# Kernel optimization log

Measured on AMD Instinct MI355X. Metric: run time of the kernel, lower is better.

## Reference

```python
import jax, jax.numpy as jnp
import numpy as np
import math

B, C, H, W = 8, 512, 32, 32
ENC = 1024
L2 = 64
NH = 8
GROUPS = 32
EPS = 1e-5

def group_norm(x, gamma, beta):
    # x: (B, C, L) GroupNorm with 32 groups (float32)
    b, c, l = x.shape
    xg = x.reshape(b, GROUPS, (c // GROUPS) * l)
    mean = xg.mean(-1, keepdims=True)
    var = xg.var(-1, keepdims=True)
    xn = ((xg - mean) * jax.lax.rsqrt(var + EPS)).reshape(b, c, l)
    return xn * gamma[None, :, None] + beta[None, :, None]

def conv1x1(w, bias, x):
    # conv_nd(1, in, out, 1): w (out, in), x (B, in, L) -> (B, out, L)
    return jnp.einsum('oc,bcl->bol', w, x) + bias[None, :, None]

def setup_inputs() -> dict:
    key = jax.random.key(0)
    ks = jax.random.split(key, 16)
    s = lambda fan_in: 1.0 / math.sqrt(fan_in)
    inp = {
        'x': jax.random.normal(ks[0], (B, C, H, W), jnp.float32),
        'xf_out': jax.random.normal(ks[1], (B, ENC, L2), jnp.float32),
        'obj_class_embedding': jax.random.normal(ks[2], (B, ENC, L2), jnp.float32),
        'obj_bbox_embedding': jax.random.normal(ks[3], (B, ENC, L2), jnp.float32),
        'image_patch_bbox_embedding': jax.random.normal(ks[4], (B, ENC, H * W), jnp.float32),
        'key_padding_mask': jax.random.bernoulli(ks[5], 0.3, (B, L2)),
        'qkv_w': jax.random.normal(ks[6], (3 * C, C), jnp.float32) * s(C),
        'qkv_b': jnp.zeros((3 * C,), jnp.float32),
        'g_qkv': jnp.ones((C,), jnp.float32),
        'b_qkv': jnp.zeros((C,), jnp.float32),
        'lc_w': jax.random.normal(ks[7], (2 * C, ENC), jnp.float32) * s(ENC),
        'lc_b': jnp.zeros((2 * C,), jnp.float32),
        'lp_w': jax.random.normal(ks[8], (C, ENC), jnp.float32) * s(ENC),
        'lp_b': jnp.zeros((C,), jnp.float32),
        'g_obj': jnp.ones((ENC,), jnp.float32),
        'b_obj': jnp.zeros((ENC,), jnp.float32),
        'g_lpos': jnp.ones((C,), jnp.float32),
        'b_lpos': jnp.zeros((C,), jnp.float32),
        'g_ipos': jnp.ones((C,), jnp.float32),
        'b_ipos': jnp.zeros((C,), jnp.float32),
        # proj_out is zero-initialized in the original (zero_module); use random
        # weights so the projection math is exercised non-trivially.
        'proj_w': jax.random.normal(ks[9], (C, C), jnp.float32) * s(C),
        'proj_b': jnp.zeros((C,), jnp.float32),
    }
    return inp

def reference(x, xf_out, obj_class_embedding, obj_bbox_embedding,
              image_patch_bbox_embedding, key_padding_mask,
              qkv_w, qkv_b, g_qkv, b_qkv, lc_w, lc_b, lp_w, lp_b,
              g_obj, b_obj, g_lpos, b_lpos, g_ipos, b_ipos, proj_w, proj_b):
    b, c, h, w = x.shape
    L1 = h * w
    d = C // NH
    xf = x.reshape(b, c, L1)

    qkv = conv1x1(qkv_w, qkv_b, group_norm(xf, g_qkv, b_qkv))  # (B, 3C, L1)
    q, k, v = jnp.split(qkv, 3, axis=1)
    q = q.reshape(b * NH, d, L1)
    k = k.reshape(b * NH, d, L1)
    v = v.reshape(b * NH, d, L1)

    ipp = group_norm(conv1x1(lp_w, lp_b, image_patch_bbox_embedding), g_ipos, b_ipos)
    ipp = ipp.reshape(b * NH, d, L1)

    q_img = jnp.concatenate([q, ipp], axis=1)  # (B*H, 2d, L1)
    k_img = jnp.concatenate([k, ipp], axis=1)

    lpe = group_norm(conv1x1(lp_w, lp_b, obj_bbox_embedding), g_lpos, b_lpos)
    lpe = lpe.reshape(b * NH, d, L2)

    lce = (xf_out + group_norm(obj_class_embedding, g_obj, b_obj)) / 2
    kl, vl = jnp.split(conv1x1(lc_w, lc_b, lce), 2, axis=1)
    kl = kl.reshape(b * NH, d, L2)
    vl = vl.reshape(b * NH, d, L2)
    k_layout = jnp.concatenate([kl, lpe], axis=1)  # (B*H, 2d, L2)

    k_mix = jnp.concatenate([k_img, k_layout], axis=2)  # (B*H, 2d, L1+L2)
    v_mix = jnp.concatenate([v, vl], axis=2)             # (B*H, d, L1+L2)

    mask = jnp.concatenate([jnp.zeros((b, L1), bool), key_padding_mask], axis=1)  # (B, L1+L2)

    scale = 1.0 / math.sqrt(math.sqrt(2 * C // NH))
    attn = jnp.einsum('bct,bcs->bts', q_img * scale, k_mix * scale)  # (B*H, L1, L1+L2)
    attn = attn.reshape(b, NH, L1, L1 + L2)
    attn = jnp.where(mask[:, None, None, :], -jnp.inf, attn)
    attn = jax.nn.softmax(attn.astype(jnp.float32), axis=-1).astype(attn.dtype)
    attn = attn.reshape(b * NH, L1, L1 + L2)

    out = jnp.einsum('bts,bcs->bct', attn, v_mix).reshape(b, C, L1)
    hproj = conv1x1(proj_w, proj_b, out)
    return (xf + hproj).reshape(b, c, h, w)
```

## Files before the change

kernel.cpp:

```cpp
#include <hip/hip_runtime.h>
#include <math.h>

#define NB 8
#define NC 512
#define NL1 1024
#define NL2 64
#define NLKV 1088
#define NENC 1024
#define EPSV 1e-5f
#define SCALE2 0.08838834764831845f
#define SCALE2Q 0.12752425f
#define DEFER_THR 11.5415603f

typedef _Float16 half8 __attribute__((ext_vector_type(8)));
typedef _Float16 half4 __attribute__((ext_vector_type(4)));
typedef __fp16 fp16x2 __attribute__((ext_vector_type(2)));
typedef float f32x4 __attribute__((ext_vector_type(4)));
typedef float f32x16 __attribute__((ext_vector_type(16)));

__device__ __forceinline__ void gload16(const _Float16* g, _Float16* l) {
  __builtin_amdgcn_global_load_lds(
      (const __attribute__((address_space(1))) void*)g,
      (__attribute__((address_space(3))) void*)l, 16, 0, 0);
}

__device__ __forceinline__ unsigned int pkrtz(float a, float b) {
  union { fp16x2 hh; unsigned int uu; } cv;
  cv.hh = __builtin_amdgcn_cvt_pkrtz(a, b);
  return cv.uu;
}

__device__ __forceinline__ float fast_exp2(float x) {
  return __builtin_amdgcn_exp2f(x);
}

__global__ __launch_bounds__(256) void k_init(
    const float* __restrict__ x, const float* __restrict__ obj,
    float* __restrict__ xm, float* __restrict__ xr,
    float* __restrict__ om, float* __restrict__ orr,
    const float* __restrict__ qkv_w, _Float16* __restrict__ w16qkv,
    const float* __restrict__ lp_w, _Float16* __restrict__ w16lp,
    const float* __restrict__ proj_w, _Float16* __restrict__ w16proj,
    const float* __restrict__ lc_w, _Float16* __restrict__ w16lc)
{
  int bid = blockIdx.x;
  if (bid < 512) {
    const float* p; float* meanp; float* rstdp; int n, bg;
    if (bid < 256) {
      bg = bid;
      int b = bg >> 5, g = bg & 31;
      p = x + ((size_t)b * 512 + (size_t)g * 16) * 1024;
      n = 16 * 1024; meanp = xm; rstdp = xr;
    } else {
      bg = bid - 256;
      int b = bg >> 5, g = bg & 31;
      p = obj + ((size_t)b * 1024 + (size_t)g * 32) * 64;
      n = 32 * 64; meanp = om; rstdp = orr;
    }
    float s = 0.f, s2 = 0.f;
    for (int i = threadIdx.x; i < n; i += 256) { float v = p[i]; s += v; s2 += v * v; }
    #pragma unroll
    for (int o = 32; o > 0; o >>= 1) { s += __shfl_down(s, o); s2 += __shfl_down(s2, o); }
    __shared__ float rs[4], rq[4];
    int lane = threadIdx.x & 63, w = threadIdx.x >> 6;
    if (lane == 0) { rs[w] = s; rq[w] = s2; }
    __syncthreads();
    if (threadIdx.x == 0) {
      float S = rs[0] + rs[1] + rs[2] + rs[3];
      float Q = rq[0] + rq[1] + rq[2] + rq[3];
      float m = S / n;
      float v = Q / n - m * m;
      if (v < 0.f) v = 0.f;
      meanp[bg] = m;
      rstdp[bg] = rsqrtf(v + EPSV);
    }
  } else {
    int cb = bid - 512;
    const float* s; _Float16* d; int i4;
    if (cb < 768)        { s = qkv_w;  d = w16qkv;  i4 = cb * 256 + threadIdx.x; }
    else if (cb < 1280)  { s = lp_w;   d = w16lp;   i4 = (cb - 768) * 256 + threadIdx.x; }
    else if (cb < 1536)  { s = proj_w; d = w16proj; i4 = (cb - 1280) * 256 + threadIdx.x; }
    else                 { s = lc_w;   d = w16lc;   i4 = (cb - 1536) * 256 + threadIdx.x; }
    float4 v = *(const float4*)&s[(size_t)i4 * 4];
// ... 70 lines not shown
      }
    }
    __syncthreads();
    int tr = threadIdx.x >> 2, c16 = (threadIdx.x & 3) * 16;
    _Float16* dst = (which == 0 ? lceT : objT) + ((size_t)b * 64 + tr) * 1024 + e0 + c16;
    *(half8*)dst = *(half8*)&tile[tr][c16];
    *(half8*)(dst + 8) = *(half8*)&tile[tr][c16 + 8];
  }
}

#define MFMA_CORE(KTOT)                                                                  \
  f32x4 acc[4][4];                                                                       \
  _Pragma("unroll") for (int i_ = 0; i_ < 4; i_++)                                       \
      _Pragma("unroll") for (int j_ = 0; j_ < 4; j_++) acc[i_][j_] = (f32x4)0.f;         \
  {                                                                                      \
    const int rsub = lane >> 3, csrc = (lane & 7) ^ rsub;                                \
    const int NT_ = (KTOT) / 64;                                                         \
    _Pragma("unroll") for (int i = 0; i < 4; i++) {                                      \
      int seg = w * 4 + i;                                                               \
      int row = seg * 8 + rsub;                                                          \
      gload16(Abase + (size_t)(m0 + row) * (KTOT) + csrc * 8, ldsA + seg * 512);         \
      gload16(Bbase + (size_t)(n0 + row) * (KTOT) + csrc * 8, ldsB + seg * 512);         \
    }                                                                                    \
    __syncthreads();                                                                     \
    int cur_ = 0;                                                                        \
    for (int t_ = 0; t_ < NT_; t_++) {                                                   \
      if (t_ + 1 < NT_) {                                                                \
        _Float16* da_ = ldsA + ((cur_ ^ 1) << 13);                                       \
        _Float16* db_ = ldsB + ((cur_ ^ 1) << 13);                                       \
        int kt = (t_ + 1) * 64;                                                          \
        _Pragma("unroll") for (int i = 0; i < 4; i++) {                                  \
          int seg = w * 4 + i;                                                           \
          int row = seg * 8 + rsub;                                                      \
          gload16(Abase + (size_t)(m0 + row) * (KTOT) + kt + csrc * 8, da_ + seg * 512); \
          gload16(Bbase + (size_t)(n0 + row) * (KTOT) + kt + csrc * 8, db_ + seg * 512); \
        }                                                                                \
      }                                                                                  \
      const char* ra_ = (const char*)(ldsA + (cur_ << 13));                              \
      const char* rb_ = (const char*)(ldsB + (cur_ << 13));                              \
      _Pragma("unroll") for (int kk = 0; kk < 2; kk++) {                                 \
        half8 af[4], bf[4];                                                              \
        _Pragma("unroll") for (int mb = 0; mb < 4; mb++) {                               \
          int row = wm + mb * 16 + l15;                                                  \
          af[mb] = *(const half8*)(ra_ + row * 128 +                                     \
                                   ((kk * 64 + lg * 16) ^ ((row & 7) << 4)));            \
        }                                                                                \
        _Pragma("unroll") for (int nb = 0; nb < 4; nb++) {                               \
          int row = wn + nb * 16 + l15;                                                  \
          bf[nb] = *(const half8*)(rb_ + row * 128 +                                     \
                                   ((kk * 64 + lg * 16) ^ ((row & 7) << 4)));            \
        }                                                                                \
        _Pragma("unroll") for (int mb = 0; mb < 4; mb++)                                 \
            _Pragma("unroll") for (int nb = 0; nb < 4; nb++)                             \
                acc[mb][nb] = __builtin_amdgcn_mfma_f32_16x16x32_f16(af[mb], bf[nb],     \
                                                                    acc[mb][nb], 0, 0, 0);\
      }                                                                                  \
      __syncthreads();                                                                   \
      cur_ ^= 1;                                                                         \
    }                                                                                    \
  }

#define MFMA_CORE_N64(KTOT)                                                              \
  f32x4 acc[4][2];                                                                       \
  _Pragma("unroll") for (int i_ = 0; i_ < 4; i_++)                                       \
      _Pragma("unroll") for (int j_ = 0; j_ < 2; j_++) acc[i_][j_] = (f32x4)0.f;         \
  {                                                                                      \
    const int rsub = lane >> 3, csrc = (lane & 7) ^ rsub;                                \
    const int NT_ = (KTOT) / 64;                                                         \
    _Pragma("unroll") for (int i = 0; i < 4; i++) {                                      \
      int seg = w * 4 + i;                                                               \
      int row = seg * 8 + rsub;                                                          \
      gload16(Abase + (size_t)(m0 + row) * (KTOT) + csrc * 8, ldsA + seg * 512);         \
    }                                                                                    \
    _Pragma("unroll") for (int i = 0; i < 2; i++) {                                      \
      int seg = w * 2 + i;                                                               \
      int row = seg * 8 + rsub;                                                          \
      gload16(Bbase + (size_t)row * (KTOT) + csrc * 8, ldsB + seg * 512);                \
    }                                                                                    \
    __syncthreads();                                                                     \
    int cur_ = 0;                                                                        \
    for (int t_ = 0; t_ < NT_; t_++) {                                                   \
      if (t_ + 1 < NT_) {                                                                \
        _Float16* da_ = ldsA + ((cur_ ^ 1) << 13);                                       \
        _Float16* db_ = ldsB + ((cur_ ^ 1) << 12);                                       \
        int kt = (t_ + 1) * 64;                                                          \
        _Pragma("unroll") for (int i = 0; i < 4; i++) {                                  \
          int seg = w * 4 + i;                                                           \
          int row = seg * 8 + rsub;                                                      \
          gload16(Abase + (size_t)(m0 + row) * (KTOT) + kt + csrc * 8, da_ + seg * 512); \
        }                                                                                \
        _Pragma("unroll") for (int i = 0; i < 2; i++) {                                  \
          int seg = w * 2 + i;                                                           \
          int row = seg * 8 + rsub;                                                      \
          gload16(Bbase + (size_t)row * (KTOT) + kt + csrc * 8, db_ + seg * 512);        \
        }                                                                                \
      }                                                                                  \
      const char* ra_ = (const char*)(ldsA + (cur_ << 13));                              \
      const char* rb_ = (const char*)(ldsB + (cur_ << 12));                              \
      _Pragma("unroll") for (int kk = 0; kk < 2; kk++) {                                 \
        half8 af[4], bf[2];                                                              \
        _Pragma("unroll") for (int mb = 0; mb < 4; mb++) {                               \
          int row = wm + mb * 16 + l15;                                                  \
          af[mb] = *(const half8*)(ra_ + row * 128 +                                     \
                                   ((kk * 64 + lg * 16) ^ ((row & 7) << 4)));            \
        }                                                                                \
        _Pragma("unroll") for (int nb = 0; nb < 2; nb++) {                               \
          int row = wn + nb * 16 + l15;                                                  \
          bf[nb] = *(const half8*)(rb_ + row * 128 +                                     \
                                   ((kk * 64 + lg * 16) ^ ((row & 7) << 4)));            \
        }                                                                                \
        _Pragma("unroll") for (int mb = 0; mb < 4; mb++)                                 \
            _Pragma("unroll") for (int nb = 0; nb < 2; nb++)                             \
                acc[mb][nb] = __builtin_amdgcn_mfma_f32_16x16x32_f16(af[mb], bf[nb],     \
                                                                    acc[mb][nb], 0, 0, 0);\
      }                                                                                  \
      __syncthreads();                                                                   \
      cur_ ^= 1;                                                                         \
    }                                                                                    \
  }

__global__ __launch_bounds__(256) void k_mfma_big(
    const _Float16* __restrict__ w16qkv, const float* __restrict__ qkv_b,
    const _Float16* __restrict__ xhatT,
    const _Float16* __restrict__ w16lp, const float* __restrict__ lp_b,
    const _Float16* __restrict__ ipbeT,
    const _Float16* __restrict__ w16lc, const float* __restrict__ lc_b,
    const _Float16* __restrict__ lceT, const _Float16* __restrict__ objT,
    const float* __restrict__ g_lpos, const float* __restrict__ b_lpos,
    _Float16* __restrict__ qT, _Float16* __restrict__ kT, _Float16* __restrict__ vT,
    _Float16* __restrict__ ipp16)
{
  __shared__ _Float16 smem[32768];
  const int bid0 = blockIdx.x;
  const int bid = (bid0 < 608) ? (bid0 + 768) : (bid0 - 608);
  const int tid = threadIdx.x, lane = tid & 63, w = tid >> 6;
  const int l15 = lane & 15, lg = lane >> 4;

  if (bid < 768) {
    const int nt = bid & 7, tt = bid >> 3;
    const int mt = tt % 12, b = tt / 12;
    const int m0 = mt * 128, n0 = nt * 128;
    _Float16* ldsA = smem;
    _Float16* ldsB = smem + 16384;
    const _Float16* Abase = w16qkv;
    const _Float16* Bbase = xhatT + (size_t)b * 1024 * 512;
    const int wm = (w >> 1) * 64, wn = (w & 1) * 64;
    MFMA_CORE(512)

    char* tb = (char*)smem;
    if (m0 < 1024) {
      const bool isq = (m0 < 512);
      const float qs = isq ? SCALE2Q : 1.f;
      #pragma unroll
      for (int mb = 0; mb < 4; mb++) {
        #pragma unroll
        for (int r = 0; r < 4; r++) {
          int mcol = wm + mb * 16 + lg * 4 + r;
          float bia = qkv_b[m0 + mcol];
          #pragma unroll
          for (int nb = 0; nb < 4; nb++) {
            int trow = wn + nb * 16 + l15;
            float val = (acc[mb][nb][r] + bia) * qs;
            *(_Float16*)(tb + ((trow * 256 + mcol * 2) ^ ((trow & 7) << 4))) = (_Float16)val;
          }
        }
      }
      __syncthreads();
      #pragma unroll
      for (int it = 0; it < 8; it++) {
        int e = it * 256 + tid;
        int trow = e >> 4, seg = e & 15;
        half8 v = *(const half8*)(tb + ((trow * 256 + seg * 16) ^ ((trow & 7) << 4)));
        if (isq) {
          int mq = m0 + seg * 8, hh = mq >> 6, dc = mq & 63;
          *(half8*)(qT + (((size_t)b * 8 + hh) * 1024 + n0 + trow) * 128 + dc) = v;
        } else {
          int mk = m0 - 512 + seg * 8, hh = mk >> 6, dc = mk & 63;
          *(half8*)(kT + (((size_t)b * 8 + hh) * 1088 + n0 + trow) * 128 + dc) = v;
        }
      }
    } else {
      #pragma unroll
      for (int mb = 0; mb < 4; mb++) {
        #pragma unroll
        for (int r = 0; r < 4; r++) {
          int mrow = wm + mb * 16 + lg * 4 + r;
          float bia = qkv_b[m0 + mrow];
          #pragma unroll
          for (int nb = 0; nb < 4; nb++) {
            int tcol = wn + nb * 16 + l15;
            *(_Float16*)(tb + ((mrow * 256 + tcol * 2) ^ ((mrow & 7) << 4))) =
                (_Float16)(acc[mb][nb][r] + bia);
          }
        }
      }
      __syncthreads();
      #pragma unroll
      for (int it = 0; it < 8; it++) {
        int e = it * 256 + tid;
        int mrow = e >> 4, seg = e & 15;
        half8 v = *(const half8*)(tb + ((mrow * 256 + seg * 16) ^ ((mrow & 7) << 4)));
        int mv = m0 - 1024 + mrow, hh = mv >> 6, dc = mv & 63;
        *(half8*)(vT + (((size_t)b * 8 + hh) * 64 + dc) * 1088 + n0 + seg * 8) = v;
      }
    }
  } else if (bid < 1280) {
    const int local = bid - 768;
    const int nt = local & 15, mt = (local >> 4) & 3, b = local >> 6;
    const int m0 = mt * 128, n0 = nt * 64;
    _Float16* ldsA = smem;
    _Float16* ldsB = smem + 16384;
    const _Float16* Abase = w16lp;
    const _Float16* Bbase = ipbeT + (size_t)b * 1024 * 1024 + (size_t)n0 * 1024;
    const int wm = (w >> 1) * 64, wn = (w & 1) * 32;
    MFMA_CORE_N64(1024)
    #pragma unroll
    for (int mb = 0; mb < 4; mb++) {
      #pragma unroll
      for (int r = 0; r < 4; r++) {
        int m = m0 + wm + mb * 16 + lg * 4 + r;
        float bia = lp_b[m];
        #pragma unroll
        for (int nb = 0; nb < 2; nb++) {
          int t = n0 + wn + nb * 16 + l15;
          ipp16[((size_t)b * NC + m) * NL1 + t] = (_Float16)(acc[mb][nb][r] + bia);
        }
      }
    }
  } else {
    const int local = bid - 1280;
    const int mt = local % 12, b = local / 12;
    const bool islc = (mt < 8);
    const int m0 = (islc ? mt : mt - 8) * 128;
    _Float16* ldsA = smem;
    _Float16* ldsB = smem + 16384;
    float (*red_s)[4] = (float(*)[4])(smem + 24576);
    float (*red_q)[4] = (float(*)[4])(smem + 24608);
    const _Float16* Abase = islc ? w16lc : w16lp;
    const float* bias = islc ? lc_b : lp_b;
    const _Float16* Bbase = (islc ? lceT : objT) + (size_t)b * 64 * 1024;
    const int wm = (w >> 1) * 64, wn = (w & 1) * 32;
    MFMA_CORE_N64(1024)

    if (islc) {
      #pragma unroll
      for (int mb = 0; mb < 4; mb++) {
        #pragma unroll
        for (int r = 0; r < 4; r++) {
          int m = m0 + wm + mb * 16 + lg * 4 + r;
          float bia = bias[m];
          #pragma unroll
          for (int nb = 0; nb < 2; nb++) {
            int l = wn + nb * 16 + l15;
// ... 43 lines not shown
      #pragma unroll
      for (int mb = 0; mb < 4; mb++) {
        float S = red_s[wbase][mb] + red_s[wbase + 1][mb];
        float Q = red_q[wbase][mb] + red_q[wbase + 1][mb];
        float mean = S * (1.f / 1024.f);
        float var = Q * (1.f / 1024.f) - mean * mean;
        if (var < 0.f) var = 0.f;
        float rstd = rsqrtf(var + EPSV);
        #pragma unroll
        for (int r = 0; r < 4; r++) {
          int c = m0 + wm + mb * 16 + lg * 4 + r;
          float ga = g_lpos[c] * rstd;
          float be = b_lpos[c] - mean * ga;
          int hh = c >> 6, dc = c & 63;
          #pragma unroll
          for (int nb = 0; nb < 2; nb++) {
            int l = wn + nb * 16 + l15;
            float xn = vals[mb][nb][r] * ga + be;
            kT[(((size_t)b * 8 + hh) * 1088 + 1024 + l) * 128 + 64 + dc] = (_Float16)xn;
          }
        }
      }
    }
  }
}

__global__ __launch_bounds__(256) void k_mfma_proj(
    const _Float16* __restrict__ Abase, const float* __restrict__ bias,
    const _Float16* __restrict__ Ball, const float* __restrict__ xin,
    float* __restrict__ out)
{
  __shared__ _Float16 smem[24576];
  _Float16* ldsA = smem;
  _Float16* ldsB = smem + 16384;
  const int b = blockIdx.z, mt = blockIdx.y, nt = blockIdx.x;
  const int m0 = mt * 128, n0 = nt * 64;
  const _Float16* Bbase = Ball + (size_t)b * 1024 * 512 + (size_t)n0 * 512;
  const int tid = threadIdx.x, lane = tid & 63, w = tid >> 6;
  const int l15 = lane & 15, lg = lane >> 4;
  const int wm = (w >> 1) * 64, wn = (w & 1) * 32;
  MFMA_CORE_N64(512)
  #pragma unroll
  for (int mb = 0; mb < 4; mb++) {
    #pragma unroll
    for (int r = 0; r < 4; r++) {
      int m = m0 + wm + mb * 16 + lg * 4 + r;
      float bia = bias[m];
      #pragma unroll
      for (int nb = 0; nb < 2; nb++) {
        int t = n0 + wn + nb * 16 + l15;
        size_t idx = ((size_t)b * NC + m) * NL1 + t;
        out[idx] = xin[idx] + acc[mb][nb][r] + bia;
      }
    }
  }
}

__global__ __launch_bounds__(256) void k_ipp_fuse(
    const _Float16* __restrict__ raw,
    const float* __restrict__ gm, const float* __restrict__ gb,
    _Float16* __restrict__ qT, _Float16* __restrict__ kT)
{
  const int g = blockIdx.x, b = blockIdx.y;
  const int tid = threadIdx.x;
  const _Float16* p = raw + ((size_t)b * 512 + (size_t)g * 16) * 1024;
  const int t0 = tid * 4;

  float4 v[16];
  float s = 0.f, s2 = 0.f;
  #pragma unroll
  for (int c = 0; c < 16; c++) {
    half4 hv = *(const half4*)&p[(size_t)c * 1024 + t0];
// ... 34 lines not shown
    #pragma unroll
    for (int c = 0; c < 8; c++) {
      float4 vc = v[c];
      float e = (j == 0) ? vc.x : (j == 1) ? vc.y : (j == 2) ? vc.z : vc.w;
      float xn = e * ga[c] + be[c];
      k0[c] = (_Float16)xn;
      q0[c] = (_Float16)(SCALE2Q * xn);
    }
    #pragma unroll
    for (int c = 8; c < 16; c++) {
      float4 vc = v[c];
      float e = (j == 0) ? vc.x : (j == 1) ? vc.y : (j == 2) ? vc.z : vc.w;
      float xn = e * ga[c] + be[c];
      k1[c - 8] = (_Float16)xn;
      q1[c - 8] = (_Float16)(SCALE2Q * xn);
    }
    _Float16* qd = qT + (bh * 1024 + t) * 128 + 64 + dcb;
    _Float16* kd = kT + (bh * 1088 + t) * 128 + 64 + dcb;
    *(half8*)qd = q0; *(half8*)(qd + 8) = q1;
    *(half8*)kd = k0; *(half8*)(kd + 8) = k1;
  }
}

__global__ __launch_bounds__(256) void k_attn_mfma(
    const _Float16* __restrict__ qT, const _Float16* __restrict__ kT,
    const _Float16* __restrict__ vT, const int* __restrict__ mask,
    _Float16* __restrict__ attnT)
{
  const int x = blockIdx.x & 7;
  const int k = blockIdx.x >> 3;
  const int bh = x + ((k >> 3) << 3);
  const int qt = k & 7;
  const int b = bh >> 3, h = bh & 7;
  const int tid = threadIdx.x;
  const int lane = tid & 63;
  const int w = tid >> 6;
  const int l31 = lane & 31;
  const int hi = lane >> 5;

  __shared__ _Float16 KsB[2 * 64 * 128];
  __shared__ _Float16 VtB[2 * 64 * 64];

  const int q = qt * 128 + w * 32 + l31;

  half8 aq[8];
  {
    const _Float16* qp = qT + ((size_t)bh * 1024 + q) * 128 + hi * 8;
    #pragma unroll
    for (int kst = 0; kst < 8; kst++) aq[kst] = *(const half8*)(qp + kst * 16);
  }

  unsigned int mbits = 0;
  {
    const int* mp = mask + b * 64;
    #pragma unroll
    for (int sb = 0; sb < 2; sb++) {
      #pragma unroll
      for (int reg = 0; reg < 16; reg++) {
        int s = sb * 32 + (reg & 3) + 8 * (reg >> 2) + 4 * hi;
        if (mp[s]) mbits |= 1u << (sb * 16 + reg);
      }
    }
  }

  f32x16 O0 = (f32x16)0.f, O1 = (f32x16)0.f;
  float m_run = -INFINITY, l_run = 0.f;

  const int kxor = (l31 & 7) << 4;
  const int ksrow_off = lane >> 4;
  const int kcsrc_base = lane & 15;
  const int vdc_off = lane >> 3;
  const int vcsrc_base = lane & 7;

#define STAGE_KV(T, KD, VD)                                                          \
  {                                                                                  \
    const int s0_ = (T) * 64;                                                        \
    _Pragma("unroll") for (int r = 0; r < 4; r++) {                                  \
      int seg = r * 4 + w;                                                           \
      int srow = seg * 4 + ksrow_off;                                                \
      int csrc = kcsrc_base ^ (srow & 7);                                            \
      gload16(kT + ((size_t)bh * 1088 + s0_ + srow) * 128 + csrc * 8, (KD) + seg * 512); \
    }                                                                                \
    _Pragma("unroll") for (int r = 0; r < 2; r++) {                                  \
      int seg = r * 4 + w;                                                           \
      int dc = seg * 8 + vdc_off;                                                    \
      int csrc = vcsrc_base ^ (dc & 7);                                              \
      gload16(vT + ((size_t)bh * 64 + dc) * 1088 + s0_ + csrc * 8, (VD) + seg * 512);  \
    }                                                                                \
  }

  STAGE_KV(0, KsB, VtB)
  asm volatile("s_waitcnt vmcnt(0)" ::: "memory");
  __builtin_amdgcn_s_barrier();

  int cur = 0;
  for (int t = 0; t < 17; t++) {
    if (t < 16) {
      _Float16* kd = KsB + ((cur ^ 1) << 13);
      _Float16* vd = VtB + ((cur ^ 1) << 12);
      STAGE_KV(t + 1, kd, vd)
    }
    const char* ksb = (const char*)(KsB + (cur << 13));
    const char* vtb = (const char*)(VtB + (cur << 12));

    f32x16 sc0 = (f32x16)0.f, sc1 = (f32x16)0.f;
    __builtin_amdgcn_s_setprio(1);
    #pragma unroll
    for (int kst = 0; kst < 8; kst++) {
      half8 kf0 = *(const half8*)(ksb + ((l31 * 256 + kst * 32 + hi * 16) ^ kxor));
      half8 kf1 = *(const half8*)(ksb + (((32 + l31) * 256 + kst * 32 + hi * 16) ^ kxor));
      sc0 = __builtin_amdgcn_mfma_f32_32x32x16_f16(kf0, aq[kst], sc0, 0, 0, 0);
      sc1 = __builtin_amdgcn_mfma_f32_32x32x16_f16(kf1, aq[kst], sc1, 0, 0, 0);
    }
    __builtin_amdgcn_s_setprio(0);

    if (t == 16) {
      #pragma unroll
      for (int i = 0; i < 16; i++) {
        if ((mbits >> i) & 1)        sc0[i] = -INFINITY;
        if ((mbits >> (16 + i)) & 1) sc1[i] = -INFINITY;
      }
    }

    float mx;
    {
      float a0 = fmaxf(fmaxf(sc0[0], sc0[1]), sc0[2]);
      float a1 = fmaxf(fmaxf(sc0[3], sc0[4]), sc0[5]);
      float a2 = fmaxf(fmaxf(sc0[6], sc0[7]), sc0[8]);
      float a3 = fmaxf(fmaxf(sc0[9], sc0[10]), sc0[11]);
      float a4 = fmaxf(fmaxf(sc0[12], sc0[13]), sc0[14]);
      float a5 = fmaxf(fmaxf(sc0[15], sc1[0]), sc1[1]);
      float a6 = fmaxf(fmaxf(sc1[2], sc1[3]), sc1[4]);
      float a7 = fmaxf(fmaxf(sc1[5], sc1[6]), sc1[7]);
      float a8 = fmaxf(fmaxf(sc1[8], sc1[9]), sc1[10]);
      float a9 = fmaxf(fmaxf(sc1[11], sc1[12]), sc1[13]);
      float aa = fmaxf(sc1[14], sc1[15]);
      float b0 = fmaxf(fmaxf(a0, a1), a2);
      float b1 = fmaxf(fmaxf(a3, a4), a5);
      float b2 = fmaxf(fmaxf(a6, a7), a8);
      float b3 = fmaxf(a9, aa);
      mx = fmaxf(fmaxf(b0, b1), fmaxf(b2, b3));
    }
    mx = fmaxf(mx, __shfl_xor(mx, 32));
    if (__all(mx <= m_run + DEFER_THR)) {
      float sum = 0.f;
      #pragma unroll
      for (int i = 0; i < 16; i++) { float p = fast_exp2(sc0[i] - m_run); sc0[i] = p; sum += p; }
      #pragma unroll
      for (int i = 0; i < 16; i++) { float p = fast_exp2(sc1[i] - m_run); sc1[i] = p; sum += p; }
      sum += __shfl_xor(sum, 32);
      l_run += sum;
    } else {
      float m_new = fmaxf(m_run, mx);
      float alpha = fast_exp2(m_run - m_new);
      float sum = 0.f;
      #pragma unroll
      for (int i = 0; i < 16; i++) { float p = fast_exp2(sc0[i] - m_new); sc0[i] = p; sum += p; }
      #pragma unroll
      for (int i = 0; i < 16; i++) { float p = fast_exp2(sc1[i] - m_new); sc1[i] = p; sum += p; }
      sum += __shfl_xor(sum, 32);
      l_run = l_run * alpha + sum;
      m_run = m_new;
      #pragma unroll
      for (int i = 0; i < 16; i++) { O0[i] *= alpha; O1[i] *= alpha; }
    }

    __builtin_amdgcn_s_setprio(1);
    #pragma unroll
    for (int sb = 0; sb < 2; sb++) {
      #pragma unroll
      for (int k2 = 0; k2 < 2; k2++) {
        const int kst = sb * 2 + k2;
        unsigned int pa0, pa1, pb0, pb1;
        if (sb == 0) {
          pa0 = pkrtz(sc0[8 * k2 + 0], sc0[8 * k2 + 1]);
          pa1 = pkrtz(sc0[8 * k2 + 2], sc0[8 * k2 + 3]);
          pb0 = pkrtz(sc0[8 * k2 + 4], sc0[8 * k2 + 5]);
          pb1 = pkrtz(sc0[8 * k2 + 6], sc0[8 * k2 + 7]);
        } else {
          pa0 = pkrtz(sc1[8 * k2 + 0], sc1[8 * k2 + 1]);
          pa1 = pkrtz(sc1[8 * k2 + 2], sc1[8 * k2 + 3]);
          pb0 = pkrtz(sc1[8 * k2 + 4], sc1[8 * k2 + 5]);
          pb1 = pkrtz(sc1[8 * k2 + 6], sc1[8 * k2 + 7]);
        }
        unsigned int keep0 = hi ? pb0 : pa0, keep1 = hi ? pb1 : pa1;
        unsigned int send0 = hi ? pa0 : pb0, send1 = hi ? pa1 : pb1;
        unsigned int recv0 = (unsigned int)__shfl_xor((int)send0, 32);
        unsigned int recv1 = (unsigned int)__shfl_xor((int)send1, 32);
        union { unsigned int u[4]; half8 hh; } pf;
        pf.u[0] = hi ? recv0 : keep0;
        pf.u[1] = hi ? recv1 : keep1;
        pf.u[2] = hi ? keep0 : recv0;
        pf.u[3] = hi ? keep1 : recv1;

        half8 vf0 = *(const half8*)(vtb + ((l31 * 128 + kst * 32 + hi * 16) ^ kxor));
        half8 vf1 = *(const half8*)(vtb + (((32 + l31) * 128 + kst * 32 + hi * 16) ^ kxor));
        O0 = __builtin_amdgcn_mfma_f32_32x32x16_f16(vf0, pf.hh, O0, 0, 0, 0);
        O1 = __builtin_amdgcn_mfma_f32_32x32x16_f16(vf1, pf.hh, O1, 0, 0, 0);
      }
    }
    __builtin_amdgcn_s_setprio(0);

    asm volatile("s_waitcnt vmcnt(0)" ::: "memory");
    __builtin_amdgcn_s_barrier();
    cur ^= 1;
  }

  float inv = 1.f / l_run;
  _Float16* op = attnT + ((size_t)b * 1024 + q) * 512 + h * 64;
  #pragma unroll
  for (int i = 0; i < 16; i += 2) {
    int dc = (i & 3) + 8 * (i >> 2) + 4 * hi;
    unsigned int c0 = pkrtz(O0[i] * inv, O0[i + 1] * inv);
    unsigned int c1 = pkrtz(O1[i] * inv, O1[i + 1] * inv);
    *(unsigned int*)(op + dc) = c0;
    *(unsigned int*)(op + 32 + dc) = c1;
  }
}

extern "C" void kernel_launch(void* const* d_in, const int* in_sizes, int n_in,
                              void* d_out, int out_size, void* d_ws, size_t ws_size,
                              hipStream_t stream) {
  const float* x         = (const float*)d_in[0];
  const float* xf_out    = (const float*)d_in[1];
  const float* obj_class = (const float*)d_in[2];
  const float* obj_bbox  = (const float*)d_in[3];
  const float* ipbe      = (const float*)d_in[4];
  const int*   mask      = (const int*)d_in[5];
// ... 19 lines not shown
  _Float16* qT      = f16b;
  _Float16* kT      = qT + 8388608;
  _Float16* vT      = kT + 8912896;
  _Float16* xhatT   = vT + 4456448;
  _Float16* ipbeT   = xhatT + 4194304;
  _Float16* attnT   = ipbeT + 8388608;
  _Float16* w16qkv  = attnT + 4194304;
  _Float16* w16lp   = w16qkv + 786432;
  _Float16* w16proj = w16lp + 524288;
  _Float16* w16lc   = w16proj + 262144;
  _Float16* lceT    = w16lc + 1048576;
  _Float16* objT    = lceT + 524288;
  _Float16* ipp16   = objT + 524288;
  float* st = (float*)(ipp16 + 4194304);
  float* xm = st, * xr = st + 256, * om = st + 512, * orr = st + 768;

  dim3 blk(256);
  k_init<<<dim3(3072), blk, 0, stream>>>(x, obj_class, xm, xr, om, orr,
                                         qkv_w, w16qkv, lp_w, w16lp, proj_w, w16proj, lc_w, w16lc);
  k_prep<<<dim3(3328), blk, 0, stream>>>(x, xm, xr, g_qkv, b_qkv, xhatT,
                                         ipbe, ipbeT,
                                         xf_out, obj_class, obj_bbox, om, orr, g_obj, b_obj,
                                         lceT, objT);
  k_mfma_big<<<dim3(1376), blk, 0, stream>>>(w16qkv, qkv_b, xhatT,
                                             w16lp, lp_b, ipbeT,
                                             w16lc, lc_b, lceT, objT,
                                             g_lpos, b_lpos,
                                             qT, kT, vT, ipp16);
  k_ipp_fuse<<<dim3(32, 8), blk, 0, stream>>>(ipp16, g_ipos, b_ipos, qT, kT);
  k_attn_mfma<<<dim3(512), blk, 0, stream>>>(qT, kT, vT, mask, attnT);
  k_mfma_proj<<<dim3(16, 4, 8), blk, 0, stream>>>(w16proj, proj_b, attnT, x, out);
}
```

Baseline: 138.2 us.

## Retile GEMMs and attention, pipeline LDS loads with vmcnt waits

```diff
diff --git a/kernel.cpp b/kernel.cpp
--- a/kernel.cpp
+++ b/kernel.cpp
@@ -17,6 +17,7 @@
 typedef __fp16 fp16x2 __attribute__((ext_vector_type(2)));
 typedef float f32x4 __attribute__((ext_vector_type(4)));
 typedef float f32x16 __attribute__((ext_vector_type(16)));
+typedef unsigned int uint32x2 __attribute__((ext_vector_type(2)));
 
 __device__ __forceinline__ void gload16(const _Float16* g, _Float16* l) {
   __builtin_amdgcn_global_load_lds(
@@ -45,7 +46,7 @@
 {
   int bid = blockIdx.x;
   if (bid < 512) {
-    const float* p; float* meanp; float* rstdp; int n, bg;
+    const float* p; float* meanp; float* rstdp; int n4, n, bg;
     if (bid < 256) {
       bg = bid;
       int b = bg >> 5, g = bg & 31;
@@ -57,8 +58,13 @@
       p = obj + ((size_t)b * 1024 + (size_t)g * 32) * 64;
       n = 32 * 64; meanp = om; rstdp = orr;
     }
+    n4 = n >> 2;
     float s = 0.f, s2 = 0.f;
-    for (int i = threadIdx.x; i < n; i += 256) { float v = p[i]; s += v; s2 += v * v; }
+    for (int i = threadIdx.x; i < n4; i += 256) {
+      float4 v = ((const float4*)p)[i];
+      s += v.x + v.y + v.z + v.w;
+      s2 += v.x * v.x + v.y * v.y + v.z * v.z + v.w * v.w;
+    }
     #pragma unroll
     for (int o = 32; o > 0; o >>= 1) { s += __shfl_down(s, o); s2 += __shfl_down(s2, o); }
     __shared__ float rs[4], rq[4];
@@ -175,7 +181,6 @@
       gload16(Abase + (size_t)(m0 + row) * (KTOT) + csrc * 8, ldsA + seg * 512);         \
       gload16(Bbase + (size_t)(n0 + row) * (KTOT) + csrc * 8, ldsB + seg * 512);         \
     }                                                                                    \
-    __syncthreads();                                                                     \
     int cur_ = 0;                                                                        \
     for (int t_ = 0; t_ < NT_; t_++) {                                                   \
       if (t_ + 1 < NT_) {                                                                \
@@ -188,7 +193,11 @@
           gload16(Abase + (size_t)(m0 + row) * (KTOT) + kt + csrc * 8, da_ + seg * 512); \
           gload16(Bbase + (size_t)(n0 + row) * (KTOT) + kt + csrc * 8, db_ + seg * 512); \
         }                                                                                \
+        asm volatile("s_waitcnt vmcnt(8)" ::: "memory");                                 \
+      } else {                                                                           \
+        asm volatile("s_waitcnt vmcnt(0)" ::: "memory");                                 \
       }                                                                                  \
+      __builtin_amdgcn_s_barrier();                                                      \
       const char* ra_ = (const char*)(ldsA + (cur_ << 13));                              \
       const char* rb_ = (const char*)(ldsB + (cur_ << 13));                              \
       _Pragma("unroll") for (int kk = 0; kk < 2; kk++) {                                 \
@@ -208,7 +217,7 @@
                 acc[mb][nb] = __builtin_amdgcn_mfma_f32_16x16x32_f16(af[mb], bf[nb],     \
                                                                     acc[mb][nb], 0, 0, 0);\
       }                                                                                  \
-      __syncthreads();                                                                   \
+      __builtin_amdgcn_s_barrier();                                                      \
       cur_ ^= 1;                                                                         \
     }                                                                                    \
   }
@@ -230,7 +239,6 @@
       int row = seg * 8 + rsub;                                                          \
       gload16(Bbase + (size_t)row * (KTOT) + csrc * 8, ldsB + seg * 512);                \
     }                                                                                    \
-    __syncthreads();                                                                     \
     int cur_ = 0;                                                                        \
     for (int t_ = 0; t_ < NT_; t_++) {                                                   \
       if (t_ + 1 < NT_) {                                                                \
@@ -247,7 +255,11 @@
           int row = seg * 8 + rsub;                                                      \
           gload16(Bbase + (size_t)row * (KTOT) + kt + csrc * 8, db_ + seg * 512);        \
         }                                                                                \
+        asm volatile("s_waitcnt vmcnt(6)" ::: "memory");                                 \
+      } else {                                                                           \
+        asm volatile("s_waitcnt vmcnt(0)" ::: "memory");                                 \
       }                                                                                  \
+      __builtin_amdgcn_s_barrier();                                                      \
       const char* ra_ = (const char*)(ldsA + (cur_ << 13));                              \
       const char* rb_ = (const char*)(ldsB + (cur_ << 12));                              \
       _Pragma("unroll") for (int kk = 0; kk < 2; kk++) {                                 \
@@ -267,7 +279,7 @@
                 acc[mb][nb] = __builtin_amdgcn_mfma_f32_16x16x32_f16(af[mb], bf[nb],     \
                                                                     acc[mb][nb], 0, 0, 0);\
       }                                                                                  \
-      __syncthreads();                                                                   \
+      __builtin_amdgcn_s_barrier();                                                      \
       cur_ ^= 1;                                                                         \
     }                                                                                    \
   }
@@ -285,88 +297,18 @@
 {
   __shared__ _Float16 smem[32768];
   const int bid0 = blockIdx.x;
-  const int bid = (bid0 < 608) ? (bid0 + 768) : (bid0 - 608);
   const int tid = threadIdx.x, lane = tid & 63, w = tid >> 6;
   const int l15 = lane & 15, lg = lane >> 4;
 
-  if (bid < 768) {
-    const int nt = bid & 7, tt = bid >> 3;
-    const int mt = tt % 12, b = tt / 12;
+  if (bid0 < 256) {
+    const int nt = bid0 & 7, mt = (bid0 >> 3) & 3, b = bid0 >> 5;
     const int m0 = mt * 128, n0 = nt * 128;
     _Float16* ldsA = smem;
     _Float16* ldsB = smem + 16384;
-    const _Float16* Abase = w16qkv;
-    const _Float16* Bbase = xhatT + (size_t)b * 1024 * 512;
+    const _Float16* Abase = w16lp;
+    const _Float16* Bbase = ipbeT + (size_t)b * 1024 * 1024;
     const int wm = (w >> 1) * 64, wn = (w & 1) * 64;
-    MFMA_CORE(512)
-
-    char* tb = (char*)smem;
-    if (m0 < 1024) {
-      const bool isq = (m0 < 512);
-      const float qs = isq ? SCALE2Q : 1.f;
-      #pragma unroll
-      for (int mb = 0; mb < 4; mb++) {
-        #pragma unroll
-        for (int r = 0; r < 4; r++) {
-          int mcol = wm + mb * 16 + lg * 4 + r;
-          float bia = qkv_b[m0 + mcol];
-          #pragma unroll
-          for (int nb = 0; nb < 4; nb++) {
-            int trow = wn + nb * 16 + l15;
-            float val = (acc[mb][nb][r] + bia) * qs;
-            *(_Float16*)(tb + ((trow * 256 + mcol * 2) ^ ((trow & 7) << 4))) = (_Float16)val;
-          }
-        }
-      }
-      __syncthreads();
-      #pragma unroll
-      for (int it = 0; it < 8; it++) {
-        int e = it * 256 + tid;
-        int trow = e >> 4, seg = e & 15;
-        half8 v = *(const half8*)(tb + ((trow * 256 + seg * 16) ^ ((trow & 7) << 4)));
-        if (isq) {
-          int mq = m0 + seg * 8, hh = mq >> 6, dc = mq & 63;
-          *(half8*)(qT + (((size_t)b * 8 + hh) * 1024 + n0 + trow) * 128 + dc) = v;
-        } else {
-          int mk = m0 - 512 + seg * 8, hh = mk >> 6, dc = mk & 63;
-          *(half8*)(kT + (((size_t)b * 8 + hh) * 1088 + n0 + trow) * 128 + dc) = v;
-        }
-      }
-    } else {
-      #pragma unroll
-      for (int mb = 0; mb < 4; mb++) {
-        #pragma unroll
-        for (int r = 0; r < 4; r++) {
-          int mrow = wm + mb * 16 + lg * 4 + r;
-          float bia = qkv_b[m0 + mrow];
-          #pragma unroll
-          for (int nb = 0; nb < 4; nb++) {
-            int tcol = wn + nb * 16 + l15;
-            *(_Float16*)(tb + ((mrow * 256 + tcol * 2) ^ ((mrow & 7) << 4))) =
-                (_Float16)(acc[mb][nb][r] + bia);
-          }
-        }
-      }
-      __syncthreads();
-      #pragma unroll
-      for (int it = 0; it < 8; it++) {
-        int e = it * 256 + tid;
-        int mrow = e >> 4, seg = e & 15;
-        half8 v = *(const half8*)(tb + ((mrow * 256 + seg * 16) ^ ((mrow & 7) << 4)));
-        int mv = m0 - 1024 + mrow, hh = mv >> 6, dc = mv & 63;
-        *(half8*)(vT + (((size_t)b * 8 + hh) * 64 + dc) * 1088 + n0 + seg * 8) = v;
-      }
-    }
-  } else if (bid < 1280) {
-    const int local = bid - 768;
-    const int nt = local & 15, mt = (local >> 4) & 3, b = local >> 6;
-    const int m0 = mt * 128, n0 = nt * 64;
-    _Float16* ldsA = smem;
-    _Float16* ldsB = smem + 16384;
-    const _Float16* Abase = w16lp;
-    const _Float16* Bbase = ipbeT + (size_t)b * 1024 * 1024 + (size_t)n0 * 1024;
-    const int wm = (w >> 1) * 64, wn = (w & 1) * 32;
-    MFMA_CORE_N64(1024)
+    MFMA_CORE(1024)
     #pragma unroll
     for (int mb = 0; mb < 4; mb++) {
       #pragma unroll
@@ -374,14 +316,14 @@
         int m = m0 + wm + mb * 16 + lg * 4 + r;
         float bia = lp_b[m];
         #pragma unroll
-        for (int nb = 0; nb < 2; nb++) {
+        for (int nb = 0; nb < 4; nb++) {
           int t = n0 + wn + nb * 16 + l15;
           ipp16[((size_t)b * NC + m) * NL1 + t] = (_Float16)(acc[mb][nb][r] + bia);
         }
       }
     }
-  } else {
-    const int local = bid - 1280;
+  } else if (bid0 < 352) {
+    const int local = bid0 - 256;
     const int mt = local % 12, b = local / 12;
     const bool islc = (mt < 8);
     const int m0 = (islc ? mt : mt - 8) * 128;
@@ -471,6 +413,75 @@
         }
       }
     }
+  } else {
+    const int bid = bid0 - 352;
+    const int nt = bid & 7, tt = bid >> 3;
+    const int mt = tt % 12, b = tt / 12;
+    const int m0 = mt * 128, n0 = nt * 128;
+    _Float16* ldsA = smem;
+    _Float16* ldsB = smem + 16384;
+    const _Float16* Abase = w16qkv;
+    const _Float16* Bbase = xhatT + (size_t)b * 1024 * 512;
+    const int wm = (w >> 1) * 64, wn = (w & 1) * 64;
+    MFMA_CORE(512)
+
+    char* tb = (char*)smem;
+    if (m0 < 1024) {
+      const bool isq = (m0 < 512);
+      const float qs = isq ? SCALE2Q : 1.f;
+      #pragma unroll
+      for (int mb = 0; mb < 4; mb++) {
+        #pragma unroll
+        for (int r = 0; r < 4; r++) {
+          int mcol = wm + mb * 16 + lg * 4 + r;
+          float bia = qkv_b[m0 + mcol];
+          #pragma unroll
+          for (int nb = 0; nb < 4; nb++) {
+            int trow = wn + nb * 16 + l15;
+            float val = (acc[mb][nb][r] + bia) * qs;
+            *(_Float16*)(tb + ((trow * 256 + mcol * 2) ^ ((trow & 7) << 4))) = (_Float16)val;
+          }
+        }
+      }
+      __syncthreads();
+      #pragma unroll
+      for (int it = 0; it < 8; it++) {
+        int e = it * 256 + tid;
+        int trow = e >> 4, seg = e & 15;
+        half8 v = *(const half8*)(tb + ((trow * 256 + seg * 16) ^ ((trow & 7) << 4)));
+        if (isq) {
+          int mq = m0 + seg * 8, hh = mq >> 6, dc = mq & 63;
+          *(half8*)(qT + (((size_t)b * 8 + hh) * 1024 + n0 + trow) * 128 + dc) = v;
+        } else {
+          int mk = m0 - 512 + seg * 8, hh = mk >> 6, dc = mk & 63;
+          *(half8*)(kT + (((size_t)b * 8 + hh) * 1088 + n0 + trow) * 128 + dc) = v;
+        }
+      }
+    } else {
+      #pragma unroll
+      for (int mb = 0; mb < 4; mb++) {
+        #pragma unroll
+        for (int r = 0; r < 4; r++) {
+          int mrow = wm + mb * 16 + lg * 4 + r;
+          float bia = qkv_b[m0 + mrow];
+          #pragma unroll
+          for (int nb = 0; nb < 4; nb++) {
+            int tcol = wn + nb * 16 + l15;
+            *(_Float16*)(tb + ((mrow * 256 + tcol * 2) ^ ((mrow & 7) << 4))) =
+                (_Float16)(acc[mb][nb][r] + bia);
+          }
+        }
+      }
+      __syncthreads();
+      #pragma unroll
+      for (int it = 0; it < 8; it++) {
+        int e = it * 256 + tid;
+        int mrow = e >> 4, seg = e & 15;
+        half8 v = *(const half8*)(tb + ((mrow * 256 + seg * 16) ^ ((mrow & 7) << 4)));
+        int mv = m0 - 1024 + mrow, hh = mv >> 6, dc = mv & 63;
+        *(half8*)(vT + (((size_t)b * 8 + hh) * 64 + dc) * 1088 + n0 + seg * 8) = v;
+      }
+    }
   }
 }
 
@@ -479,16 +490,16 @@
     const _Float16* __restrict__ Ball, const float* __restrict__ xin,
     float* __restrict__ out)
 {
-  __shared__ _Float16 smem[24576];
+  __shared__ _Float16 smem[32768];
   _Float16* ldsA = smem;
   _Float16* ldsB = smem + 16384;
   const int b = blockIdx.z, mt = blockIdx.y, nt = blockIdx.x;
-  const int m0 = mt * 128, n0 = nt * 64;
-  const _Float16* Bbase = Ball + (size_t)b * 1024 * 512 + (size_t)n0 * 512;
+  const int m0 = mt * 128, n0 = nt * 128;
+  const _Float16* Bbase = Ball + (size_t)b * 1024 * 512;
   const int tid = threadIdx.x, lane = tid & 63, w = tid >> 6;
   const int l15 = lane & 15, lg = lane >> 4;
-  const int wm = (w >> 1) * 64, wn = (w & 1) * 32;
-  MFMA_CORE_N64(512)
+  const int wm = (w >> 1) * 64, wn = (w & 1) * 64;
+  MFMA_CORE(512)
   #pragma unroll
   for (int mb = 0; mb < 4; mb++) {
     #pragma unroll
@@ -496,7 +507,7 @@
       int m = m0 + wm + mb * 16 + lg * 4 + r;
       float bia = bias[m];
       #pragma unroll
-      for (int nb = 0; nb < 2; nb++) {
+      for (int nb = 0; nb < 4; nb++) {
         int t = n0 + wn + nb * 16 + l15;
         size_t idx = ((size_t)b * NC + m) * NL1 + t;
         out[idx] = xin[idx] + acc[mb][nb][r] + bia;
@@ -577,15 +588,14 @@
   }
 }
 
-__global__ __launch_bounds__(256) void k_attn_mfma(
+__global__ __launch_bounds__(512, 1) void k_attn_mfma(
     const _Float16* __restrict__ qT, const _Float16* __restrict__ kT,
     const _Float16* __restrict__ vT, const int* __restrict__ mask,
     _Float16* __restrict__ attnT)
 {
-  const int x = blockIdx.x & 7;
-  const int k = blockIdx.x >> 3;
-  const int bh = x + ((k >> 3) << 3);
-  const int qt = k & 7;
+  const int bid = blockIdx.x;
+  const int bh = bid & 63;
+  const int qt = bid >> 6;
   const int b = bh >> 3, h = bh & 7;
   const int tid = threadIdx.x;
   const int lane = tid & 63;
@@ -593,10 +603,10 @@
   const int l31 = lane & 31;
   const int hi = lane >> 5;
 
-  __shared__ _Float16 KsB[2 * 64 * 128];
-  __shared__ _Float16 VtB[2 * 64 * 64];
-
-  const int q = qt * 128 + w * 32 + l31;
+  __shared__ _Float16 KsB[2 * 128 * 128];
+  __shared__ _Float16 VtB[3 * 64 * 128];
+
+  const int q = qt * 256 + w * 32 + l31;
 
   half8 aq[8];
   {
@@ -622,143 +632,156 @@
   float m_run = -INFINITY, l_run = 0.f;
 
   const int kxor = (l31 & 7) << 4;
-  const int ksrow_off = lane >> 4;
-  const int kcsrc_base = lane & 15;
-  const int vdc_off = lane >> 3;
-  const int vcsrc_base = lane & 7;
+  const int row_off = lane >> 4;
+  const int blk_base = lane & 15;
 
 #define STAGE_KV(T, KD, VD)                                                          \
   {                                                                                  \
-    const int s0_ = (T) * 64;                                                        \
+    const int s0_ = (T) * 128;                                                       \
     _Pragma("unroll") for (int r = 0; r < 4; r++) {                                  \
-      int seg = r * 4 + w;                                                           \
-      int srow = seg * 4 + ksrow_off;                                                \
-      int csrc = kcsrc_base ^ (srow & 7);                                            \
+      int seg = r * 8 + w;                                                           \
+      int srow = seg * 4 + row_off;                                                  \
+      int csrc = blk_base ^ (srow & 7);                                              \
       gload16(kT + ((size_t)bh * 1088 + s0_ + srow) * 128 + csrc * 8, (KD) + seg * 512); \
     }                                                                                \
     _Pragma("unroll") for (int r = 0; r < 2; r++) {                                  \
-      int seg = r * 4 + w;                                                           \
-      int dc = seg * 8 + vdc_off;                                                    \
-      int csrc = vcsrc_base ^ (dc & 7);                                              \
+      int seg = r * 8 + w;                                                           \
+      int dc = seg * 4 + row_off;                                                    \
+      int csrc = blk_base ^ (dc & 7);                                                \
       gload16(vT + ((size_t)bh * 64 + dc) * 1088 + s0_ + csrc * 8, (VD) + seg * 512);  \
     }                                                                                \
   }
+
+#define XHALF_FMAX(OUTV, INV)                                                        \
+  { unsigned int xi_ = __float_as_uint(INV);                                         \
+    uint32x2 xr_ = __builtin_amdgcn_permlane32_swap(xi_, xi_, false, false);         \
+    OUTV = fmaxf(__uint_as_float(xr_.x), __uint_as_float(xr_.y)); }
+#define XHALF_ADD(OUTV, INV)                                                         \
+  { unsigned int xi_ = __float_as_uint(INV);                                         \
+    uint32x2 xr_ = __builtin_amdgcn_permlane32_swap(xi_, xi_, false, false);         \
+    OUTV = __uint_as_float(xr_.x) + __uint_as_float(xr_.y); }
+
+#define MAX32(OUTV, P0, P1)                                                          \
+  { float a0 = fmaxf(fmaxf(P0[0], P0[1]), P0[2]);                                    \
+    float a1 = fmaxf(fmaxf(P0[3], P0[4]), P0[5]);                                    \
+    float a2 = fmaxf(fmaxf(P0[6], P0[7]), P0[8]);                                    \
+    float a3 = fmaxf(fmaxf(P0[9], P0[10]), P0[11]);                                  \
+    float a4 = fmaxf(fmaxf(P0[12], P0[13]), P0[14]);                                 \
+    float a5 = fmaxf(fmaxf(P0[15], P1[0]), P1[1]);                                   \
+    float a6 = fmaxf(fmaxf(P1[2], P1[3]), P1[4]);                                    \
+    float a7 = fmaxf(fmaxf(P1[5], P1[6]), P1[7]);                                    \
+    float a8 = fmaxf(fmaxf(P1[8], P1[9]), P1[10]);                                   \
+    float a9 = fmaxf(fmaxf(P1[11], P1[12]), P1[13]);                                 \
+    float aa = fmaxf(P1[14], P1[15]);                                                \
+    float b0 = fmaxf(fmaxf(a0, a1), a2);                                             \
+    float b1 = fmaxf(fmaxf(a3, a4), a5);                                             \
+    float b2 = fmaxf(fmaxf(a6, a7), a8);                                             \
+    float b3 = fmaxf(a9, aa);                                                        \
+    OUTV = fmaxf(fmaxf(b0, b1), fmaxf(b2, b3)); }
+
+#define EXP16(P, M, SUM)                                                             \
+  _Pragma("unroll") for (int i = 0; i < 16; i++) {                                   \
+    float p_ = fast_exp2(P[i] - (M)); P[i] = p_; SUM += p_; }
+
+#define PACK_G(PFU, SC, K2)                                                          \
+  { unsigned int pa0 = pkrtz(SC[8 * (K2) + 0], SC[8 * (K2) + 1]);                    \
+    unsigned int pa1 = pkrtz(SC[8 * (K2) + 2], SC[8 * (K2) + 3]);                    \
+    unsigned int pb0 = pkrtz(SC[8 * (K2) + 4], SC[8 * (K2) + 5]);                    \
+    unsigned int pb1 = pkrtz(SC[8 * (K2) + 6], SC[8 * (K2) + 7]);                    \
+    uint32x2 r0_ = __builtin_amdgcn_permlane32_swap(pa0, pb0, false, false);         \
+    uint32x2 r1_ = __builtin_amdgcn_permlane32_swap(pa1, pb1, false, false);         \
+    PFU.u[0] = r0_.x; PFU.u[1] = r1_.x; PFU.u[2] = r0_.y; PFU.u[3] = r1_.y; }
 
   STAGE_KV(0, KsB, VtB)
   asm volatile("s_waitcnt vmcnt(0)" ::: "memory");
   __builtin_amdgcn_s_barrier();
 
-  int cur = 0;
-  for (int t = 0; t < 17; t++) {
-    if (t < 16) {
-      _Float16* kd = KsB + ((cur ^ 1) << 13);
-      _Float16* vd = VtB + ((cur ^ 1) << 12);
-      STAGE_KV(t + 1, kd, vd)
-    }
-    const char* ksb = (const char*)(KsB + (cur << 13));
-    const char* vtb = (const char*)(VtB + (cur << 12));
+  for (int t = 0; t <= 8; t++) {
+    if (t < 8) {
+      STAGE_KV(t + 1, KsB + ((t + 1) & 1) * 16384, VtB + ((t + 1) % 3) * 8192)
+    }
+    const char* ksb_ = (const char*)(KsB + (t & 1) * 16384);
 
     f32x16 sc0 = (f32x16)0.f, sc1 = (f32x16)0.f;
+    f32x16 sc2 = (f32x16)0.f, sc3 = (f32x16)0.f;
+    const bool full = (t < 8);
     __builtin_amdgcn_s_setprio(1);
     #pragma unroll
     for (int kst = 0; kst < 8; kst++) {
-      half8 kf0 = *(const half8*)(ksb + ((l31 * 256 + kst * 32 + hi * 16) ^ kxor));
-      half8 kf1 = *(const half8*)(ksb + (((32 + l31) * 256 + kst * 32 + hi * 16) ^ kxor));
+      half8 kf0 = *(const half8*)(ksb_ + ((l31 * 256 + kst * 32 + hi * 16) ^ kxor));
+      half8 kf1 = *(const half8*)(ksb_ + (((32 + l31) * 256 + kst * 32 + hi * 16) ^ kxor));
       sc0 = __builtin_amdgcn_mfma_f32_32x32x16_f16(kf0, aq[kst], sc0, 0, 0, 0);
       sc1 = __builtin_amdgcn_mfma_f32_32x32x16_f16(kf1, aq[kst], sc1, 0, 0, 0);
+      if (full) {
+        half8 kf2 = *(const half8*)(ksb_ + (((64 + l31) * 256 + kst * 32 + hi * 16) ^ kxor));
+        half8 kf3 = *(const half8*)(ksb_ + (((96 + l31) * 256 + kst * 32 + hi * 16) ^ kxor));
+        sc2 = __builtin_amdgcn_mfma_f32_32x32x16_f16(kf2, aq[kst], sc2, 0, 0, 0);
+        sc3 = __builtin_amdgcn_mfma_f32_32x32x16_f16(kf3, aq[kst], sc3, 0, 0, 0);
+      }
     }
     __builtin_amdgcn_s_setprio(0);
 
-    if (t == 16) {
+    if (!full) {
       #pragma unroll
       for (int i = 0; i < 16; i++) {
         if ((mbits >> i) & 1)        sc0[i] = -INFINITY;
         if ((mbits >> (16 + i)) & 1) sc1[i] = -INFINITY;
-      }
-    }
-
-    float mx;
-    {
-      float a0 = fmaxf(fmaxf(sc0[0], sc0[1]), sc0[2]);
-      float a1 = fmaxf(fmaxf(sc0[3], sc0[4]), sc0[5]);
-      float a2 = fmaxf(fmaxf(sc0[6], sc0[7]), sc0[8]);
-      float a3 = fmaxf(fmaxf(sc0[9], sc0[10]), sc0[11]);
-      float a4 = fmaxf(fmaxf(sc0[12], sc0[13]), sc0[14]);
-      float a5 = fmaxf(fmaxf(sc0[15], sc1[0]), sc1[1]);
-      float a6 = fmaxf(fmaxf(sc1[2], sc1[3]), sc1[4]);
-      float a7 = fmaxf(fmaxf(sc1[5], sc1[6]), sc1[7]);
-      float a8 = fmaxf(fmaxf(sc1[8], sc1[9]), sc1[10]);
-      float a9 = fmaxf(fmaxf(sc1[11], sc1[12]), sc1[13]);
-      float aa = fmaxf(sc1[14], sc1[15]);
-      float b0 = fmaxf(fmaxf(a0, a1), a2);
-      float b1 = fmaxf(fmaxf(a3, a4), a5);
-      float b2 = fmaxf(fmaxf(a6, a7), a8);
-      float b3 = fmaxf(a9, aa);
-      mx = fmaxf(fmaxf(b0, b1), fmaxf(b2, b3));
-    }
-    mx = fmaxf(mx, __shfl_xor(mx, 32));
+        sc2[i] = -INFINITY;
+        sc3[i] = -INFINITY;
+      }
+    }
+
+    float mx01, mx23, mx;
+    MAX32(mx01, sc0, sc1)
+    if (full) { MAX32(mx23, sc2, sc3) mx = fmaxf(mx01, mx23); }
+    else mx = mx01;
+    XHALF_FMAX(mx, mx)
     if (__all(mx <= m_run + DEFER_THR)) {
       float sum = 0.f;
-      #pragma unroll
-      for (int i = 0; i < 16; i++) { float p = fast_exp2(sc0[i] - m_run); sc0[i] = p; sum += p; }
-      #pragma unroll
-      for (int i = 0; i < 16; i++) { float p = fast_exp2(sc1[i] - m_run); sc1[i] = p; sum += p; }
-      sum += __shfl_xor(sum, 32);
+      EXP16(sc0, m_run, sum)
+      EXP16(sc1, m_run, sum)
+      if (full) { EXP16(sc2, m_run, sum) EXP16(sc3, m_run, sum) }
+      XHALF_ADD(sum, sum)
       l_run += sum;
     } else {
       float m_new = fmaxf(m_run, mx);
       float alpha = fast_exp2(m_run - m_new);
       float sum = 0.f;
-      #pragma unroll
-      for (int i = 0; i < 16; i++) { float p = fast_exp2(sc0[i] - m_new); sc0[i] = p; sum += p; }
-      #pragma unroll
-      for (int i = 0; i < 16; i++) { float p = fast_exp2(sc1[i] - m_new); sc1[i] = p; sum += p; }
-      sum += __shfl_xor(sum, 32);
+      EXP16(sc0, m_new, sum)
+      EXP16(sc1, m_new, sum)
+      if (full) { EXP16(sc2, m_new, sum) EXP16(sc3, m_new, sum) }
+      XHALF_ADD(sum, sum)
       l_run = l_run * alpha + sum;
       m_run = m_new;
       #pragma unroll
       for (int i = 0; i < 16; i++) { O0[i] *= alpha; O1[i] *= alpha; }
     }
 
+    const char* vtb_ = (const char*)(VtB + (t % 3) * 8192);
     __builtin_amdgcn_s_setprio(1);
     #pragma unroll
-    for (int sb = 0; sb < 2; sb++) {
+    for (int g = 0; g < 4; g++) {
+      if (g >= 2 && !full) continue;
       #pragma unroll
       for (int k2 = 0; k2 < 2; k2++) {
-        const int kst = sb * 2 + k2;
-        unsigned int pa0, pa1, pb0, pb1;
-        if (sb == 0) {
-          pa0 = pkrtz(sc0[8 * k2 + 0], sc0[8 * k2 + 1]);
-          pa1 = pkrtz(sc0[8 * k2 + 2], sc0[8 * k2 + 3]);
-          pb0 = pkrtz(sc0[8 * k2 + 4], sc0[8 * k2 + 5]);
-          pb1 = pkrtz(sc0[8 * k2 + 6], sc0[8 * k2 + 7]);
-        } else {
-          pa0 = pkrtz(sc1[8 * k2 + 0], sc1[8 * k2 + 1]);
-          pa1 = pkrtz(sc1[8 * k2 + 2], sc1[8 * k2 + 3]);
-          pb0 = pkrtz(sc1[8 * k2 + 4], sc1[8 * k2 + 5]);
-          pb1 = pkrtz(sc1[8 * k2 + 6], sc1[8 * k2 + 7]);
-        }
-        unsigned int keep0 = hi ? pb0 : pa0, keep1 = hi ? pb1 : pa1;
-        unsigned int send0 = hi ? pa0 : pb0, send1 = hi ? pa1 : pb1;
-        unsigned int recv0 = (unsigned int)__shfl_xor((int)send0, 32);
-        unsigned int recv1 = (unsigned int)__shfl_xor((int)send1, 32);
+        const int kst = g * 2 + k2;
         union { unsigned int u[4]; half8 hh; } pf;
-        pf.u[0] = hi ? recv0 : keep0;
-        pf.u[1] = hi ? recv1 : keep1;
-        pf.u[2] = hi ? keep0 : recv0;
-        pf.u[3] = hi ? keep1 : recv1;
-
-        half8 vf0 = *(const half8*)(vtb + ((l31 * 128 + kst * 32 + hi * 16) ^ kxor));
-        half8 vf1 = *(const half8*)(vtb + (((32 + l31) * 128 + kst * 32 + hi * 16) ^ kxor));
+        if (g == 0)      { PACK_G(pf, sc0, k2) }
+        else if (g == 1) { PACK_G(pf, sc1, k2) }
+        else if (g == 2) { PACK_G(pf, sc2, k2) }
+        else             { PACK_G(pf, sc3, k2) }
+        half8 vf0 = *(const half8*)(vtb_ + ((l31 * 256 + kst * 32 + hi * 16) ^ kxor));
+        half8 vf1 = *(const half8*)(vtb_ + (((32 + l31) * 256 + kst * 32 + hi * 16) ^ kxor));
         O0 = __builtin_amdgcn_mfma_f32_32x32x16_f16(vf0, pf.hh, O0, 0, 0, 0);
         O1 = __builtin_amdgcn_mfma_f32_32x32x16_f16(vf1, pf.hh, O1, 0, 0, 0);
       }
     }
     __builtin_amdgcn_s_setprio(0);
 
-    asm volatile("s_waitcnt vmcnt(0)" ::: "memory");
-    __builtin_amdgcn_s_barrier();
-    cur ^= 1;
+    if (t < 8) {
+      asm volatile("s_waitcnt vmcnt(0)" ::: "memory");
+      __builtin_amdgcn_s_barrier();
+    }
   }
 
   float inv = 1.f / l_run;
@@ -824,12 +847,12 @@
                                          ipbe, ipbeT,
                                          xf_out, obj_class, obj_bbox, om, orr, g_obj, b_obj,
                                          lceT, objT);
-  k_mfma_big<<<dim3(1376), blk, 0, stream>>>(w16qkv, qkv_b, xhatT,
+  k_mfma_big<<<dim3(1120), blk, 0, stream>>>(w16qkv, qkv_b, xhatT,
                                              w16lp, lp_b, ipbeT,
                                              w16lc, lc_b, lceT, objT,
                                              g_lpos, b_lpos,
                                              qT, kT, vT, ipp16);
   k_ipp_fuse<<<dim3(32, 8), blk, 0, stream>>>(ipp16, g_ipos, b_ipos, qT, kT);
-  k_attn_mfma<<<dim3(512), blk, 0, stream>>>(qT, kT, vT, mask, attnT);
-  k_mfma_proj<<<dim3(16, 4, 8), blk, 0, stream>>>(w16proj, proj_b, attnT, x, out);
-}
+  k_attn_mfma<<<dim3(256), dim3(512), 0, stream>>>(qT, kT, vT, mask, attnT);
+  k_mfma_proj<<<dim3(8, 4, 8), blk, 0, stream>>>(w16proj, proj_b, attnT, x, out);
+}
```

After: 149.9 us. +8.5%, slower.
